# Kernel tuning notes

Measured on AMD Instinct MI355X. Metric: run time of the kernel, lower is better.

## Reference

```python
import jax, jax.numpy as jnp
import numpy as np

D_IN = 4096
NUM_LATENTS = 65536
GROUP_DIM = 64
GROUP_MUL = 4
IN_GROUPS = D_IN // GROUP_DIM      # 64
OUT_GROUPS = NUM_LATENTS // GROUP_DIM  # 1024
TOKENS = 2048


def setup_inputs() -> dict:
    key = jax.random.key(0)
    k1, k2, k3, k4, k5 = jax.random.split(key, 5)
    x = jax.random.normal(k1, (TOKENS, D_IN), dtype=jnp.float32)
    # nn.Linear default init ~ U(-1/sqrt(d), 1/sqrt(d)); scale randn similarly for stability
    s = 1.0 / np.sqrt(D_IN)
    pre_w = jax.random.normal(k2, (D_IN, D_IN), dtype=jnp.float32) * s
    pre_b = jax.random.normal(k3, (D_IN,), dtype=jnp.float32) * s
    inner = jax.random.normal(k4, (GROUP_MUL, IN_GROUPS, GROUP_DIM, GROUP_DIM), dtype=jnp.float32)
    outer = jax.random.normal(k5, (OUT_GROUPS, GROUP_MUL, IN_GROUPS), dtype=jnp.float32)
    return {"x": x, "pre_w": pre_w, "pre_b": pre_b, "inner": inner, "outer": outer}


def reference(x, pre_w, pre_b, inner, outer):
    # pre: dense linear, x @ W^T + b  -> (tokens, d_in)
    h = x @ pre_w.T + pre_b
    # unflatten last dim into (in_groups, group_dim)
    h = h.reshape(h.shape[0], IN_GROUPS, GROUP_DIM)  # (b, i, x)
    # block-diagonal mix: (b,i,x) x (m,i,x,y) -> (b,m,i,y)
    t = jnp.einsum('bix,mixy->bmiy', h, inner)
    # low-rank outer combine: (b,m,i,y) x (o,m,i) -> (b,o,y)
    out = jnp.einsum('bmiy,omi->boy', t, outer)
    # flatten (o, y) -> num_latents; note: module's _bias is unused in forward
    return out.reshape(out.shape[0], NUM_LATENTS)
```

## Files before the change

### kernel.cpp

```cpp
#include <hip/hip_runtime.h>
#include <hip/hip_bf16.h>
#include <stdint.h>

#define D_IN 4096
#define TOKENS 2048
#define NUM_LATENTS 65536
#define GROUP_DIM 64
#define GROUP_MUL 4
#define IN_GROUPS 64
#define OUT_GROUPS 1024
#define KMID 256

typedef __attribute__((ext_vector_type(8))) short short8;
typedef __attribute__((ext_vector_type(4))) float f32x4;

struct alignas(8)  US4 { unsigned short v[4]; };

#define FLAT_BLOCKS 24832

__device__ inline unsigned short f2bf(float f) {
    union { float f; unsigned u; } w{f};
    unsigned r = w.u + 0x7fffu + ((w.u >> 16) & 1u);
    return (unsigned short)(r >> 16);
}

__device__ inline void gload_lds16(const void* g, void* l) {
    __builtin_amdgcn_global_load_lds(
        (const __attribute__((address_space(1))) void*)g,
        (__attribute__((address_space(3))) void*)l, 16, 0, 0);
}

__device__ inline int SWZ(int y, int k) {
    return ((y << 9) + (k << 1)) ^ ((((y & 7) ^ ((y >> 3) & 7)) << 4));
}

__global__ __launch_bounds__(256) void cvt_all(
    const float* __restrict__ w, const float* __restrict__ x,
    const float* __restrict__ outer, const float* __restrict__ inner,
    unsigned short* __restrict__ w_bf, unsigned short* __restrict__ x_bf,
    unsigned short* __restrict__ o_bf, unsigned short* __restrict__ it_bf) {
    __shared__ float tl[64][65];
    int blk = blockIdx.x;
    const int tid = threadIdx.x;
    if (blk >= FLAT_BLOCKS) {
        blk -= FLAT_BLOCKS;
        const float* src = inner + (size_t)blk * 4096;
        #pragma unroll
        for (int p = 0; p < 4; ++p) {
            int idx = p * 1024 + tid * 4;
            int xx = idx >> 6, y = idx & 63;
            f32x4 v = *(const f32x4*)(src + idx);
            #pragma unroll
            for (int j = 0; j < 4; ++j) tl[xx][y + j] = v[j];
        }
        __syncthreads();
        unsigned short* dst = it_bf + (size_t)blk * 4096;
        #pragma unroll
        for (int p = 0; p < 4; ++p) {
            int idx = p * 1024 + tid * 4;
            int y = idx >> 6, x0 = idx & 63;
            US4 o;
            #pragma unroll
            for (int j = 0; j < 4; ++j) o.v[j] = f2bf(tl[x0 + j][y]);
            *(US4*)(dst + y * 64 + (x0 ^ ((y & 7) << 3))) = o;
        }
        return;
    }
    int s = blk * 256 + tid;
    if (s < 4194304) {
        f32x4 v = *(const f32x4*)(w + (size_t)s * 4);
        US4 o;
        #pragma unroll
        for (int j = 0; j < 4; ++j) o.v[j] = f2bf(v[j]);
        *(US4*)(w_bf + (size_t)s * 4) = o;
    } else if (s < 6291456) {
        int t = s - 4194304;
        f32x4 v = *(const f32x4*)(x + (size_t)t * 4);
        US4 o;
        #pragma unroll
        for (int j = 0; j < 4; ++j) o.v[j] = f2bf(v[j]);
        *(US4*)(x_bf + (size_t)t * 4) = o;
    } else {
        int t0 = (s - 6291456) * 4;
        int o = t0 >> 8, r = t0 & 255, m = r >> 6, i = r & 63;
        f32x4 v = *(const f32x4*)(outer + t0);
        #pragma unroll
        for (int j = 0; j < 4; ++j)
            o_bf[(o << 8) + (i + j) * 4 + m] = f2bf(v[j]);
    }
}

__global__ __launch_bounds__(256, 2) void gemm_fused(
    const unsigned short* __restrict__ A,
    const unsigned short* __restrict__ B,
    const float* __restrict__ bias,
    const unsigned short* __restrict__ IT,
    unsigned short* __restrict__ T)
{
    __shared__ unsigned short smem[40960];
    unsigned short* inn = smem + 32768;

    const int tid = threadIdx.x;
    const int lane = tid & 63;
    const int w = tid >> 6;
    const int wm = w >> 1, wn = w & 1;
    int bx = blockIdx.x;
    bx = (bx & 7) * 64 + (bx >> 3);
    const int m0 = (bx & 15) * 128;
    const int n0 = (bx >> 4) * 128;
    const int i0 = n0 >> 6;

    const int lr = lane & 15;
    const int hi = lane >> 4;
    const int lk = hi * 8;

    f32x4 acc[4][4] = {};

    auto STAGE = [&](int buf, int k0) {
        #pragma unroll
        for (int c = 0; c < 4; ++c) {
            int f = c * 2048 + tid * 8;
            int r = f >> 6;
            int colsw = ((((f >> 3) & 7) ^ (r & 7)) << 3);
            gload_lds16(A + (size_t)(m0 + r) * D_IN + k0 + colsw, smem + buf * 16384 + f);
            gload_lds16(B + (size_t)(n0 + r) * D_IN + k0 + colsw, smem + buf * 16384 + 8192 + f);
        }
    };
    auto COMPUTE = [&](int buf) {
        const unsigned short* as = smem + buf * 16384;
        const unsigned short* bs = as + 8192;
        #pragma unroll
        for (int kk = 0; kk < 2; ++kk) {
            short8 a[4], b[4];
            #pragma unroll
            for (int mi = 0; mi < 4; ++mi) {
                int row = wm * 64 + mi * 16 + lr;
                a[mi] = *(const short8*)(as + (row << 6) + ((((kk << 2) + hi) ^ (lr & 7)) << 3));
            }
            #pragma unroll
            for (int ni = 0; ni < 4; ++ni) {
                int row = wn * 64 + ni * 16 + lr;
                b[ni] = *(const short8*)(bs + (row << 6) + ((((kk << 2) + hi) ^ (lr & 7)) << 3));
            }
            __builtin_amdgcn_s_setprio(1);
            #pragma unroll
            for (int mi = 0; mi < 4; ++mi)
                #pragma unroll
                for (int ni = 0; ni < 4; ++ni)
                    acc[mi][ni] = __builtin_amdgcn_mfma_f32_16x16x32_bf16(b[ni], a[mi], acc[mi][ni], 0, 0, 0);
            __builtin_amdgcn_s_setprio(0);
        }
    };

    STAGE(0, 0);
    #pragma unroll 1
    for (int t = 0; t < 64; ++t) {
        asm volatile("s_waitcnt vmcnt(0)" ::: "memory");
        __builtin_amdgcn_s_barrier();
        __builtin_amdgcn_sched_barrier(0);
        if (t < 63) STAGE((t + 1) & 1, (t + 1) * 64);
        COMPUTE(t & 1);
        __builtin_amdgcn_sched_barrier(0);
    }

    #pragma unroll
    for (int ni = 0; ni < 4; ++ni) {
        int col0 = wn * 64 + ni * 16 + hi * 4;
        f32x4 bv = *(const f32x4*)(bias + n0 + col0);
        #pragma unroll
        for (int mi = 0; mi < 4; ++mi) {
            int tok = wm * 64 + mi * 16 + lr;
            US4 o;
            #pragma unroll
            for (int j = 0; j < 4; ++j) o.v[j] = f2bf(acc[mi][ni][j] + bv[j]);
            *(US4*)(smem + tok * 128 + (col0 ^ ((tok & 7) << 3))) = o;
        }
    }

    for (int m = 0; m < 4; ++m) {
        #pragma unroll
        for (int c = 0; c < 4; ++c) {
            int e = c * 2048 + tid * 8;
            int i_loc = e >> 12, rem = e & 4095;
            gload_lds16(IT + ((size_t)(m * 64 + i0 + i_loc) << 12) + rem, inn + e);
        }
        asm volatile("s_waitcnt vmcnt(0)" ::: "memory");
        __syncthreads();

        f32x4 acc2[4][4] = {};
        #pragma unroll
        for (int kk = 0; kk < 2; ++kk) {
            short8 a[4], b2[4];
            #pragma unroll
            for (int mi = 0; mi < 4; ++mi) {
                int tok = wm * 64 + mi * 16 + lr;
                a[mi] = *(const short8*)(smem + tok * 128 + ((wn * 64 + kk * 32 + lk) ^ ((tok & 7) << 3)));
            }
            #pragma unroll
            for (int ni = 0; ni < 4; ++ni) {
                int y = ni * 16 + lr;
                b2[ni] = *(const short8*)(inn + wn * 4096 + y * 64 + ((kk * 32 + lk) ^ ((y & 7) << 3)));
            }
            #pragma unroll
            for (int mi = 0; mi < 4; ++mi)
                #pragma unroll
                for (int ni = 0; ni < 4; ++ni)
                    acc2[mi][ni] = __builtin_amdgcn_mfma_f32_16x16x32_bf16(b2[ni], a[mi], acc2[mi][ni], 0, 0, 0);
        }

        const int kp = (i0 + wn) * 4 + m;
        #pragma unroll
        for (int mi = 0; mi < 4; ++mi) {
            int tok = m0 + wm * 64 + mi * 16 + lr;
            unsigned short* trow = T + ((size_t)tok * KMID + kp) * 64;
            #pragma unroll
            for (int ni = 0; ni < 4; ++ni) {
                int y0 = ni * 16 + hi * 4;
                US4 o;
                #pragma unroll
                for (int j = 0; j < 4; ++j) o.v[j] = f2bf(acc2[mi][ni][j]);
                *(US4*)(trow + y0) = o;
            }
        }
        __syncthreads();
    }
}

__global__ __launch_bounds__(512) void stage3(
    const unsigned short* __restrict__ T,
    const unsigned short* __restrict__ Ob,
    float* __restrict__ out)
{
    __shared__ char ts[32768];
    const int tid = threadIdx.x;
    const int lane = tid & 63;
    const int w = tid >> 6;
    int bx = blockIdx.x;
    const int b = (bx & 7) * 256 + (bx >> 3);
    const int lr = lane & 15;
    const int hi = lane >> 4;

    {
        const unsigned short* src = T + (size_t)b * (KMID * 64);
        #pragma unroll
        for (int c = 0; c < 4; ++c) {
            int e = c * 4096 + tid * 8;
            int k = e >> 6, y = e & 63;
            short8 v = __builtin_nontemporal_load((const short8*)(src + e));
            #pragma unroll
            for (int j = 0; j < 8; ++j)
                *(unsigned short*)(ts + SWZ(y + j, k)) = (unsigned short)v[j];
        }
    }
    __syncthreads();

    const int o_base = w * 128;
    f32x4 acc[4][8] = {};
    for (int kt = 0; kt < 8; ++kt) {
        short8 tf[4], of[8];
        #pragma unroll
        for (int ni = 0; ni < 4; ++ni)
            tf[ni] = *(const short8*)(ts + SWZ(ni * 16 + lr, kt * 32 + hi * 8));
        #pragma unroll
        for (int mi = 0; mi < 8; ++mi)
            of[mi] = *(const short8*)(Ob + ((size_t)(o_base + mi * 16 + lr) << 8) + kt * 32 + hi * 8);
        #pragma unroll
        for (int ni = 0; ni < 4; ++ni)
            #pragma unroll
            for (int mi = 0; mi < 8; ++mi)
                acc[ni][mi] = __builtin_amdgcn_mfma_f32_16x16x32_bf16(tf[ni], of[mi], acc[ni][mi], 0, 0, 0);
    }

    float* ob = out + (size_t)b * NUM_LATENTS;
    #pragma unroll
    for (int ni = 0; ni < 4; ++ni) {
        #pragma unroll
        for (int mi = 0; mi < 8; ++mi) {
            int o = o_base + mi * 16 + lr;
            int y = ni * 16 + hi * 4;
            __builtin_nontemporal_store(acc[ni][mi], (f32x4*)(ob + (o << 6) + y));
        }
    }
}

extern "C" void kernel_launch(void* const* d_in, const int* in_sizes, int n_in,
                              void* d_out, int out_size, void* d_ws, size_t ws_size,
                              hipStream_t stream) {
    const float* x     = (const float*)d_in[0];
    const float* pre_w = (const float*)d_in[1];
    const float* pre_b = (const float*)d_in[2];
    const float* inner = (const float*)d_in[3];
    const float* outer = (const float*)d_in[4];
    float* out = (float*)d_out;

    char* ws = (char*)d_ws;
    unsigned short* x_bf = (unsigned short*)ws;  ws += (size_t)TOKENS * D_IN * 2;
    unsigned short* w_bf = (unsigned short*)ws;  ws += (size_t)D_IN * D_IN * 2;
    unsigned short* o_bf = (unsigned short*)ws;  ws += (size_t)OUT_GROUPS * KMID * 2;
    unsigned short* t_bf = (unsigned short*)ws;  ws += (size_t)TOKENS * KMID * 64 * 2;
    unsigned short* it_bf = (unsigned short*)ws; ws += (size_t)GROUP_MUL * IN_GROUPS * 64 * 64 * 2;

    cvt_all<<<FLAT_BLOCKS + GROUP_MUL * IN_GROUPS, 256, 0, stream>>>(
        pre_w, x, outer, inner, w_bf, x_bf, o_bf, it_bf);

    gemm_fused<<<512, 256, 0, stream>>>(x_bf, w_bf, pre_b, it_bf, t_bf);
    stage3<<<2048, 512, 0, stream>>>(t_bf, o_bf, out);
}
```

Before: 313.3 us.

## Widen GEMM tile to 128x256 with 8 waves and phased LDS/MFMA interleave

The fused GEMM kernel moves from 128x128 tiles with 4 waves to 128x256 tiles with 8 waves, so each staged A tile is reused across twice as many output columns and 256 blocks are launched instead of 512. The inner loop is split into four barrier-separated phases that interleave global-to-LDS staging of the next K slice with LDS reads and MFMA bursts, aiming to overlap memory and compute. LDS use rises to 96KB per block and the grid drops to 256 blocks, which may underfill the CUs. The extra barriers and reduced occupancy could also offset the gain from reuse.

```diff
diff --git a/kernel.cpp b/kernel.cpp
--- a/kernel.cpp
+++ b/kernel.cpp
@@ -5,10 +5,8 @@
 #define D_IN 4096
 #define TOKENS 2048
 #define NUM_LATENTS 65536
-#define GROUP_DIM 64
 #define GROUP_MUL 4
 #define IN_GROUPS 64
-#define OUT_GROUPS 1024
 #define KMID 256
 
 typedef __attribute__((ext_vector_type(8))) short short8;
@@ -90,24 +88,24 @@
     }
 }
 
-__global__ __launch_bounds__(256, 2) void gemm_fused(
+__global__ __launch_bounds__(512, 2) void gemm_fused(
     const unsigned short* __restrict__ A,
     const unsigned short* __restrict__ B,
     const float* __restrict__ bias,
     const unsigned short* __restrict__ IT,
     unsigned short* __restrict__ T)
 {
-    __shared__ unsigned short smem[40960];
-    unsigned short* inn = smem + 32768;
+    __shared__ unsigned short smem[49152];
 
     const int tid = threadIdx.x;
     const int lane = tid & 63;
     const int w = tid >> 6;
-    const int wm = w >> 1, wn = w & 1;
+    const int wm = w >> 2;
+    const int wn = w & 3;
     int bx = blockIdx.x;
-    bx = (bx & 7) * 64 + (bx >> 3);
-    const int m0 = (bx & 15) * 128;
-    const int n0 = (bx >> 4) * 128;
+    const int logical = (bx & 7) * 32 + (bx >> 3);
+    const int m0 = (logical & 15) * 128;
+    const int n0 = (logical >> 4) * 256;
     const int i0 = n0 >> 6;
 
     const int lr = lane & 15;
@@ -116,51 +114,88 @@
 
     f32x4 acc[4][4] = {};
 
-    auto STAGE = [&](int buf, int k0) {
-        #pragma unroll
-        for (int c = 0; c < 4; ++c) {
-            int f = c * 2048 + tid * 8;
+    auto STAGE_A = [&](unsigned short* As, int k0) {
+        #pragma unroll
+        for (int c = 0; c < 2; ++c) {
+            int f = c * 4096 + tid * 8;
             int r = f >> 6;
             int colsw = ((((f >> 3) & 7) ^ (r & 7)) << 3);
-            gload_lds16(A + (size_t)(m0 + r) * D_IN + k0 + colsw, smem + buf * 16384 + f);
-            gload_lds16(B + (size_t)(n0 + r) * D_IN + k0 + colsw, smem + buf * 16384 + 8192 + f);
+            gload_lds16(A + (size_t)(m0 + r) * D_IN + k0 + colsw, As + f);
         }
     };
-    auto COMPUTE = [&](int buf) {
-        const unsigned short* as = smem + buf * 16384;
-        const unsigned short* bs = as + 8192;
-        #pragma unroll
-        for (int kk = 0; kk < 2; ++kk) {
-            short8 a[4], b[4];
-            #pragma unroll
-            for (int mi = 0; mi < 4; ++mi) {
-                int row = wm * 64 + mi * 16 + lr;
-                a[mi] = *(const short8*)(as + (row << 6) + ((((kk << 2) + hi) ^ (lr & 7)) << 3));
-            }
-            #pragma unroll
-            for (int ni = 0; ni < 4; ++ni) {
-                int row = wn * 64 + ni * 16 + lr;
-                b[ni] = *(const short8*)(bs + (row << 6) + ((((kk << 2) + hi) ^ (lr & 7)) << 3));
-            }
-            __builtin_amdgcn_s_setprio(1);
-            #pragma unroll
-            for (int mi = 0; mi < 4; ++mi)
-                #pragma unroll
-                for (int ni = 0; ni < 4; ++ni)
-                    acc[mi][ni] = __builtin_amdgcn_mfma_f32_16x16x32_bf16(b[ni], a[mi], acc[mi][ni], 0, 0, 0);
-            __builtin_amdgcn_s_setprio(0);
+    auto STAGE_B = [&](unsigned short* Bs, int k0, int c0) {
+        #pragma unroll
+        for (int c = 0; c < 2; ++c) {
+            int f = (c0 + c) * 4096 + tid * 8;
+            int r = f >> 6;
+            int colsw = ((((f >> 3) & 7) ^ (r & 7)) << 3);
+            gload_lds16(B + (size_t)(n0 + r) * D_IN + k0 + colsw, Bs + f);
         }
     };
 
-    STAGE(0, 0);
+    STAGE_A(smem, 0);
+    STAGE_B(smem + 8192, 0, 0);
+    STAGE_B(smem + 8192, 0, 2);
+
+    short8 a0, a1, a2, a3, b0, b1, b2, b3;
+    #define RD_A(dst, mi, kk, as) { int row = wm * 64 + (mi) * 16 + lr; \
+        dst = *(const short8*)((as) + (row << 6) + ((((kk << 2) + hi) ^ (lr & 7)) << 3)); }
+    #define RD_B(dst, ni, kk, bs) { int row = wn * 64 + (ni) * 16 + lr; \
+        dst = *(const short8*)((bs) + (row << 6) + ((((kk << 2) + hi) ^ (lr & 7)) << 3)); }
+    #define MF(mi, ni, bb, aa) acc[mi][ni] = __builtin_amdgcn_mfma_f32_16x16x32_bf16(bb, aa, acc[mi][ni], 0, 0, 0);
+    #define PHASE_TAIL \
+        __builtin_amdgcn_s_barrier(); \
+        asm volatile("s_waitcnt lgkmcnt(0)" ::: "memory"); \
+        __builtin_amdgcn_sched_barrier(0);
+    #define PHASE_END \
+        __builtin_amdgcn_s_setprio(0); \
+        __builtin_amdgcn_s_barrier(); \
+        __builtin_amdgcn_sched_barrier(0);
+
     #pragma unroll 1
     for (int t = 0; t < 64; ++t) {
+        unsigned short* As = smem + (t & 1) * 24576;
+        unsigned short* Bs = As + 8192;
+        unsigned short* Asn = smem + ((t & 1) ^ 1) * 24576;
+        unsigned short* Bsn = Asn + 8192;
+        const int kn = (t + 1) * 64;
+
         asm volatile("s_waitcnt vmcnt(0)" ::: "memory");
         __builtin_amdgcn_s_barrier();
         __builtin_amdgcn_sched_barrier(0);
-        if (t < 63) STAGE((t + 1) & 1, (t + 1) * 64);
-        COMPUTE(t & 1);
-        __builtin_amdgcn_sched_barrier(0);
+
+        if (t < 63) STAGE_A(Asn, kn);
+        RD_A(a0, 0, 0, As) RD_A(a1, 1, 0, As) RD_A(a2, 2, 0, As) RD_A(a3, 3, 0, As)
+        RD_B(b0, 0, 0, Bs) RD_B(b1, 1, 0, Bs)
+        PHASE_TAIL
+        __builtin_amdgcn_s_setprio(1);
+        MF(0,0,b0,a0) MF(1,0,b0,a1) MF(2,0,b0,a2) MF(3,0,b0,a3)
+        MF(0,1,b1,a0) MF(1,1,b1,a1) MF(2,1,b1,a2) MF(3,1,b1,a3)
+        PHASE_END
+
+        if (t < 63) STAGE_B(Bsn, kn, 0);
+        RD_B(b2, 2, 0, Bs) RD_B(b3, 3, 0, Bs)
+        PHASE_TAIL
+        __builtin_amdgcn_s_setprio(1);
+        MF(0,2,b2,a0) MF(1,2,b2,a1) MF(2,2,b2,a2) MF(3,2,b2,a3)
+        MF(0,3,b3,a0) MF(1,3,b3,a1) MF(2,3,b3,a2) MF(3,3,b3,a3)
+        PHASE_END
+
+        if (t < 63) STAGE_B(Bsn, kn, 2);
+        RD_A(a0, 0, 1, As) RD_A(a1, 1, 1, As) RD_A(a2, 2, 1, As) RD_A(a3, 3, 1, As)
+        RD_B(b0, 0, 1, Bs) RD_B(b1, 1, 1, Bs)
+        PHASE_TAIL
+        __builtin_amdgcn_s_setprio(1);
+        MF(0,0,b0,a0) MF(1,0,b0,a1) MF(2,0,b0,a2) MF(3,0,b0,a3)
+        MF(0,1,b1,a0) MF(1,1,b1,a1) MF(2,1,b1,a2) MF(3,1,b1,a3)
+        PHASE_END
+
+        RD_B(b2, 2, 1, Bs) RD_B(b3, 3, 1, Bs)
+        PHASE_TAIL
+        __builtin_amdgcn_s_setprio(1);
+        MF(0,2,b2,a0) MF(1,2,b2,a1) MF(2,2,b2,a2) MF(3,2,b2,a3)
+        MF(0,3,b3,a0) MF(1,3,b3,a1) MF(2,3,b3,a2) MF(3,3,b3,a3)
+        PHASE_END
     }
 
     #pragma unroll
@@ -173,16 +208,17 @@
             US4 o;
             #pragma unroll
             for (int j = 0; j < 4; ++j) o.v[j] = f2bf(acc[mi][ni][j] + bv[j]);
-            *(US4*)(smem + tok * 128 + (col0 ^ ((tok & 7) << 3))) = o;
-        }
-    }
-
+            *(US4*)(smem + tok * 256 + (col0 ^ ((tok & 7) << 3))) = o;
+        }
+    }
+
+    unsigned short* inn = smem + 32768;
     for (int m = 0; m < 4; ++m) {
         #pragma unroll
         for (int c = 0; c < 4; ++c) {
-            int e = c * 2048 + tid * 8;
-            int i_loc = e >> 12, rem = e & 4095;
-            gload_lds16(IT + ((size_t)(m * 64 + i0 + i_loc) << 12) + rem, inn + e);
+            int e = c * 4096 + tid * 8;
+            int i_l = e >> 12, rem = e & 4095;
+            gload_lds16(IT + ((size_t)(m * 64 + i0 + i_l) << 12) + rem, inn + e);
         }
         asm volatile("s_waitcnt vmcnt(0)" ::: "memory");
         __syncthreads();
@@ -190,22 +226,22 @@
         f32x4 acc2[4][4] = {};
         #pragma unroll
         for (int kk = 0; kk < 2; ++kk) {
-            short8 a[4], b2[4];
+            short8 a[4], b2v[4];
             #pragma unroll
             for (int mi = 0; mi < 4; ++mi) {
                 int tok = wm * 64 + mi * 16 + lr;
-                a[mi] = *(const short8*)(smem + tok * 128 + ((wn * 64 + kk * 32 + lk) ^ ((tok & 7) << 3)));
+                a[mi] = *(const short8*)(smem + tok * 256 + ((wn * 64 + kk * 32 + lk) ^ ((tok & 7) << 3)));
             }
             #pragma unroll
             for (int ni = 0; ni < 4; ++ni) {
                 int y = ni * 16 + lr;
-                b2[ni] = *(const short8*)(inn + wn * 4096 + y * 64 + ((kk * 32 + lk) ^ ((y & 7) << 3)));
+                b2v[ni] = *(const short8*)(inn + wn * 4096 + y * 64 + ((kk * 32 + lk) ^ ((y & 7) << 3)));
             }
             #pragma unroll
             for (int mi = 0; mi < 4; ++mi)
                 #pragma unroll
                 for (int ni = 0; ni < 4; ++ni)
-                    acc2[mi][ni] = __builtin_amdgcn_mfma_f32_16x16x32_bf16(b2[ni], a[mi], acc2[mi][ni], 0, 0, 0);
+                    acc2[mi][ni] = __builtin_amdgcn_mfma_f32_16x16x32_bf16(b2v[ni], a[mi], acc2[mi][ni], 0, 0, 0);
         }
 
         const int kp = (i0 + wn) * 4 + m;
@@ -224,6 +260,11 @@
         }
         __syncthreads();
     }
+    #undef RD_A
+    #undef RD_B
+    #undef MF
+    #undef PHASE_TAIL
+    #undef PHASE_END
 }
 
 __global__ __launch_bounds__(512) void stage3(
@@ -296,13 +337,13 @@
     char* ws = (char*)d_ws;
     unsigned short* x_bf = (unsigned short*)ws;  ws += (size_t)TOKENS * D_IN * 2;
     unsigned short* w_bf = (unsigned short*)ws;  ws += (size_t)D_IN * D_IN * 2;
-    unsigned short* o_bf = (unsigned short*)ws;  ws += (size_t)OUT_GROUPS * KMID * 2;
+    unsigned short* o_bf = (unsigned short*)ws;  ws += (size_t)1024 * KMID * 2;
     unsigned short* t_bf = (unsigned short*)ws;  ws += (size_t)TOKENS * KMID * 64 * 2;
     unsigned short* it_bf = (unsigned short*)ws; ws += (size_t)GROUP_MUL * IN_GROUPS * 64 * 64 * 2;
 
     cvt_all<<<FLAT_BLOCKS + GROUP_MUL * IN_GROUPS, 256, 0, stream>>>(
         pre_w, x, outer, inner, w_bf, x_bf, o_bf, it_bf);
 
-    gemm_fused<<<512, 256, 0, stream>>>(x_bf, w_bf, pre_b, it_bf, t_bf);
+    gemm_fused<<<256, 512, 0, stream>>>(x_bf, w_bf, pre_b, it_bf, t_bf);
     stage3<<<2048, 512, 0, stream>>>(t_bf, o_bf, out);
 }
```

Result: no change. 315.4 us (+0.7%).
